# Performance work log

Measured on AMD Instinct MI355X. Metric: run time of the kernel, lower is better.

The kernel has to match this reference:

```python
import jax, jax.numpy as jnp
import numpy as np

N_NODES = 50000
N_EDGES = 500000
D = 128
VOCAB = 10000
OUT = 64
LAYERS = 3
N_GRAPHS = 512


def setup_inputs() -> dict:
    key = jax.random.key(0)
    ks = jax.random.split(key, 10)
    nodes = jax.random.randint(ks[0], (N_NODES,), 0, VOCAB)
    edges = jax.random.randint(ks[1], (2, N_EDGES), 0, N_NODES)
    indices = jax.random.randint(ks[2], (N_NODES,), 0, N_GRAPHS)
    emb = jax.random.normal(ks[3], (VOCAB, D), dtype=jnp.float32) * 0.02
    W0 = jax.random.normal(ks[4], (LAYERS, D, D), dtype=jnp.float32) * (1.0 / np.sqrt(D))
    W1 = jax.random.normal(ks[5], (LAYERS, D, D), dtype=jnp.float32) * (1.0 / np.sqrt(D))
    W2 = jax.random.normal(ks[6], (LAYERS, D, D), dtype=jnp.float32) * (1.0 / np.sqrt(D))
    Wout = jax.random.normal(ks[7], (2 * D, OUT), dtype=jnp.float32) * (1.0 / np.sqrt(2 * D))
    bout = jnp.zeros((OUT,), dtype=jnp.float32)
    return {"nodes": nodes, "edges": edges, "indices": indices, "num_graphs": N_GRAPHS,
            "emb": emb, "W0": W0, "W1": W1, "W2": W2, "Wout": Wout, "bout": bout}


def reference(nodes, edges, indices, num_graphs, emb, W0, W1, W2, Wout, bout):
    n = nodes.shape[0]
    h = emb[nodes]  # [N, D]; Dropout(0.5) is identity in eval mode
    src, dst = edges[0], edges[1]
    seg = jnp.concatenate([dst, src])  # message destinations, [2E]
    deg = jax.ops.segment_sum(jnp.ones_like(seg, dtype=h.dtype), seg, num_segments=n)
    deg = jnp.maximum(deg, 1.0)[:, None]
    for l in range(W0.shape[0]):
        # per-edge linear on gathered endpoints (nn.Linear: x @ W.T)
        m = jnp.concatenate([h[src] @ W1[l].T, h[dst] @ W2[l].T], axis=0)  # [2E, D]
        msg = jax.ops.segment_sum(m, seg, num_segments=n) / deg  # scatter_mean
        h = jax.nn.relu(h @ W0[l].T + msg)
    # graph pooling: scatter_mean + scatter_max
    cnt = jax.ops.segment_sum(jnp.ones((n,), h.dtype), indices, num_segments=num_graphs)
    mean = jax.ops.segment_sum(h, indices, num_segments=num_graphs) / jnp.maximum(cnt, 1.0)[:, None]
    mx = jax.ops.segment_max(h, indices, num_segments=num_graphs)
    mx = jnp.where(jnp.isfinite(mx), mx, 0.0)  # empty segments -> 0 (torch_scatter default)
    v = jnp.concatenate([mean, mx], axis=1)  # [G, 2D]
    return v @ Wout + bout
```

## Files before the change

kernel.cpp:

```cpp
#include <hip/hip_runtime.h>
#include <hip/hip_bf16.h>

#define D 128
#define GRAPHS 512
#define OUTD 64
#define NR 64
#define NSL 16
#define NSCAN (NR * NSL)
#define LRANGE 800

typedef _Float16 half4v __attribute__((ext_vector_type(4)));
typedef _Float16 half8v __attribute__((ext_vector_type(8)));
typedef float float4v __attribute__((ext_vector_type(4)));
typedef float float8v __attribute__((ext_vector_type(8)));
typedef unsigned short u16;

__global__ __launch_bounds__(256) void prep_kernel(
    const int* __restrict__ edges, const int* __restrict__ indices,
    int* __restrict__ pc_in, int* __restrict__ pc_out, int* __restrict__ pc_g,
    const int* __restrict__ nodes, const float* __restrict__ emb,
    _Float16* __restrict__ h,
    const float* __restrict__ W0, const float* __restrict__ W1,
    const float* __restrict__ W2, _Float16* __restrict__ Wpk,
    int E, int n) {
    int tid = threadIdx.x;
    if (blockIdx.x < NSCAN) {
        __shared__ int lin[LRANGE];
        __shared__ int lout[LRANGE];
        int s = blockIdx.x >> 6;
        int r = blockIdx.x & (NR - 1);
        int range = (n + NR - 1) / NR;
        int lo = r * range, hi = min(lo + range, n), len = hi - lo;
        for (int j = tid; j < len; j += 256) { lin[j] = 0; lout[j] = 0; }
        __syncthreads();
        int echunk = (((E + NSL - 1) / NSL) + 3) & ~3;
        int elo = s * echunk, ehi = min(elo + echunk, E);
#define HI(arr, k) { unsigned r_ = (unsigned)((k) - lo); if (r_ < (unsigned)len) atomicAdd(&arr[r_], 1); }
        {
            const int4* s4 = (const int4*)(edges + elo);
            const int4* d4 = (const int4*)(edges + E + elo);
            int m4 = (ehi - elo) >> 2;
            for (int it = tid; it < m4; it += 256) {
                int4 sv = s4[it], dv = d4[it];
                HI(lin, dv.x) HI(lin, dv.y) HI(lin, dv.z) HI(lin, dv.w)
                HI(lout, sv.x) HI(lout, sv.y) HI(lout, sv.z) HI(lout, sv.w)
            }
            for (int e = elo + m4 * 4 + tid; e < ehi; e += 256) {
                HI(lin, edges[E + e])
                HI(lout, edges[e])
            }
        }
#undef HI
        __syncthreads();
        for (int j = tid; j < len; j += 256) {
            pc_in[s * n + lo + j] = lin[j];
            pc_out[s * n + lo + j] = lout[j];
        }
        int grange = (GRAPHS + NR - 1) / NR;
        int glo = r * grange, ghi = min(glo + grange, GRAPHS), glen = ghi - glo;
        __syncthreads();
        for (int j = tid; j < glen; j += 256) lin[j] = 0;
        __syncthreads();
        int ichunk = (((n + NSL - 1) / NSL) + 3) & ~3;
        int ilo = s * ichunk, ihi = min(ilo + ichunk, n);
#define GH(k) { unsigned r_ = (unsigned)((k) - glo); if (r_ < (unsigned)glen) atomicAdd(&lin[r_], 1); }
        {
            const int4* i4 = (const int4*)(indices + ilo);
            int g4 = (ihi - ilo) >> 2;
            for (int it = tid; it < g4; it += 256) {
                int4 v = i4[it];
                GH(v.x) GH(v.y) GH(v.z) GH(v.w)
            }
            for (int e = ilo + g4 * 4 + tid; e < ihi; e += 256) GH(indices[e])
        }
#undef GH
        __syncthreads();
        for (int j = tid; j < glen; j += 256) pc_g[s * GRAPHS + glo + j] = lin[j];
        return;
    }
    int i = (blockIdx.x - NSCAN) * 256 + tid;
    if (i < n * 16) {
        int v = i >> 4, q = i & 15;
        const float4* e4 = (const float4*)emb + (size_t)nodes[v] * 32 + q * 2;
        float4 f0 = e4[0];
        float4 f1 = e4[1];
        half8v o = {(_Float16)f0.x, (_Float16)f0.y, (_Float16)f0.z, (_Float16)f0.w,
                    (_Float16)f1.x, (_Float16)f1.y, (_Float16)f1.z, (_Float16)f1.w};
        ((half8v*)h)[i] = o;
    }
    if (i < 36864) {
        int j4 = (i & 1) * 4;
        int t = i >> 1;
        int lane = t & 63; t >>= 6;
        int nf = t & 7;   t >>= 3;
        int ks = t & 3;   t >>= 2;
        int src = t % 3;
        int l = t / 3;
        const float* W = (src == 0 ? W0 : (src == 1 ? W1 : W2)) + l * D * D;
        int col = nf * 16 + (lane & 15);
        int k = ks * 32 + (lane >> 4) * 8 + j4;
        float4 f = *(const float4*)&W[col * D + k];
        half4v o = {(_Float16)f.x, (_Float16)f.y, (_Float16)f.z, (_Float16)f.w};
        _Float16* dst = Wpk + ((size_t)(((l * 3 + src) * 4 + ks) * 8 + nf) * 64 + lane) * 8 + j4;
        *(half4v*)dst = o;
    }
}

__global__ __launch_bounds__(256) void offsets_kernel(
    const int* __restrict__ pc_in, int* __restrict__ o16_in,
    int* __restrict__ off_in, int* __restrict__ tot_in,
    const int* __restrict__ pc_out, int* __restrict__ o16_out,
    int* __restrict__ off_out, int* __restrict__ tot_out,
    const int* __restrict__ pc_g, int* __restrict__ o16_g,
    int* __restrict__ goff, int* __restrict__ gtot,
    int* totals, int n) {
    __shared__ int ws[8];
    int tid = threadIdx.x;
    int lane = tid & 63, wid = tid >> 6;
    int i = blockIdx.x * 256 + tid;

#define SCAN16(pc, o16, off, tot_arr, total, len)                          \
    do {                                                                   \
        int part_[NSL]; int tot_ = 0;                                      \
        if (i < (len)) {                                                   \
            _Pragma("unroll") for (int k_ = 0; k_ < NSL; ++k_) {           \
                part_[k_] = (pc)[k_ * (len) + i]; tot_ += part_[k_];       \
            }                                                              \
        }                                                                  \
        int v_ = tot_;                                                     \
        _Pragma("unroll") for (int d_ = 1; d_ < 64; d_ <<= 1) {            \
            int t_ = __shfl_up(v_, d_, 64);                                \
            if (lane >= d_) v_ += t_;                                      \
        }                                                                  \
        if (lane == 63) ws[wid] = v_;                                      \
        __syncthreads();                                                   \
        if (tid == 0) {                                                    \
            int s_ = 0;                                                    \
            for (int k_ = 0; k_ < 4; ++k_) { int t_ = ws[k_]; ws[k_] = s_; s_ += t_; } \
            ws[4] = atomicAdd((total), s_);                                \
        }                                                                  \
        __syncthreads();                                                   \
        if (i < (len)) {                                                   \
            int run_ = ws[4] + ws[wid] + v_ - tot_;                        \
            (off)[i] = run_; (tot_arr)[i] = tot_;                          \
            _Pragma("unroll") for (int k_ = 0; k_ < NSL; ++k_) {           \
                (o16)[k_ * (len) + i] = run_; run_ += part_[k_];           \
            }                                                              \
        }                                                                  \
        __syncthreads();                                                   \
    } while (0)

    SCAN16(pc_in, o16_in, off_in, tot_in, &totals[0], n);
    SCAN16(pc_out, o16_out, off_out, tot_out, &totals[1], n);
    if (blockIdx.x < (GRAPHS + 255) / 256)
        SCAN16(pc_g, o16_g, goff, gtot, &totals[2], GRAPHS);
#undef SCAN16
}

__global__ __launch_bounds__(256) void fill_kernel(
    const int* __restrict__ edges, const int* __restrict__ indices,
    const int* __restrict__ o16_in, const int* __restrict__ o16_out,
    const int* __restrict__ o16_g,
    u16* __restrict__ csr_in, u16* __restrict__ csr_out, u16* __restrict__ glist,
    int E, int n) {
    __shared__ int cin[LRANGE];
    __shared__ int cout[LRANGE];
    __shared__ int cg[8];
    int tid = threadIdx.x;
    int s = blockIdx.x >> 6;
    int r = blockIdx.x & (NR - 1);
    int range = (n + NR - 1) / NR;
    int lo = r * range, hi = min(lo + range, n), len = hi - lo;
    int grange = (GRAPHS + NR - 1) / NR;
    int glo = r * grange, ghi = min(glo + grange, GRAPHS), glen = ghi - glo;
    for (int j = tid; j < len; j += 256) {
        cin[j] = o16_in[s * n + lo + j];
        cout[j] = o16_out[s * n + lo + j];
    }
    for (int j = tid; j < glen; j += 256) cg[j] = o16_g[s * GRAPHS + glo + j];
    __syncthreads();

    int echunk = (((E + NSL - 1) / NSL) + 3) & ~3;
    int elo = s * echunk, ehi = min(elo + echunk, E);
#define FIN(k, pay) { unsigned r_ = (unsigned)((k) - lo); if (r_ < (unsigned)len) { \
        int p_ = atomicAdd(&cin[r_], 1); csr_in[p_] = (u16)(pay); } }
#define FOUT(k, pay) { unsigned r_ = (unsigned)((k) - lo); if (r_ < (unsigned)len) { \
        int p_ = atomicAdd(&cout[r_], 1); csr_out[p_] = (u16)(pay); } }
    {
        const int4* s4 = (const int4*)(edges + elo);
        const int4* d4 = (const int4*)(edges + E + elo);
        int m4 = (ehi - elo) >> 2;
        for (int it = tid; it < m4; it += 256) {
            int4 sv = s4[it], dv = d4[it];
            FIN(dv.x, sv.x) FIN(dv.y, sv.y) FIN(dv.z, sv.z) FIN(dv.w, sv.w)
            FOUT(sv.x, dv.x) FOUT(sv.y, dv.y) FOUT(sv.z, dv.z) FOUT(sv.w, dv.w)
        }
        for (int e = elo + m4 * 4 + tid; e < ehi; e += 256) {
            int se = edges[e], de = edges[E + e];
            FIN(de, se)
            FOUT(se, de)
        }
    }
#undef FIN
#undef FOUT
#define FG(g, vv) { unsigned r_ = (unsigned)((g) - glo); if (r_ < (unsigned)glen) { \
        int p_ = atomicAdd(&cg[r_], 1); glist[p_] = (u16)(vv); } }
    {
        int ichunk = (((n + NSL - 1) / NSL) + 3) & ~3;
        int ilo = s * ichunk, ihi = min(ilo + ichunk, n);
        const int4* i4 = (const int4*)(indices + ilo);
        int g4 = (ihi - ilo) >> 2;
        for (int it = tid; it < g4; it += 256) {
            int4 v = i4[it];
            int e = ilo + it * 4;
            FG(v.x, e) FG(v.y, e + 1) FG(v.z, e + 2) FG(v.w, e + 3)
        }
        for (int e = ilo + g4 * 4 + tid; e < ihi; e += 256) FG(indices[e], e)
    }
#undef FG
}

__global__ __launch_bounds__(256) void aggregate_kernel(
    const _Float16* __restrict__ h,
    const u16* __restrict__ csr_in, const int* __restrict__ off_in, const int* __restrict__ cnt_in,
    const u16* __restrict__ csr_out, const int* __restrict__ off_out, const int* __restrict__ cnt_out,
    _Float16* __restrict__ agg1, _Float16* __restrict__ agg2, int n) {
    int grp = threadIdx.x >> 4;
    int lane = threadIdx.x & 15;
    int v = blockIdx.x * 16 + grp;
    if (v >= n) return;
    int s1 = off_in[v], c1 = cnt_in[v];
    int s2 = off_out[v], c2 = cnt_out[v];
    float invd = 1.0f / fmaxf((float)(c1 + c2), 1.0f);
    const half8v* h8 = (const half8v*)h;

    float8v a1 = {0.f, 0.f, 0.f, 0.f, 0.f, 0.f, 0.f, 0.f};
    int i = 0;
    for (; i + 4 <= c1; i += 4) {
        int u0 = csr_in[s1 + i], u1 = csr_in[s1 + i + 1];
        int u2 = csr_in[s1 + i + 2], u3 = csr_in[s1 + i + 3];
        half8v p0 = h8[u0 * 16 + lane];
        half8v p1 = h8[u1 * 16 + lane];
        half8v p2 = h8[u2 * 16 + lane];
        half8v p3 = h8[u3 * 16 + lane];
        a1 += (__builtin_convertvector(p0, float8v) + __builtin_convertvector(p1, float8v)) +
              (__builtin_convertvector(p2, float8v) + __builtin_convertvector(p3, float8v));
    }
    for (; i < c1; ++i)
        a1 += __builtin_convertvector(h8[csr_in[s1 + i] * 16 + lane], float8v);

    float8v a2 = {0.f, 0.f, 0.f, 0.f, 0.f, 0.f, 0.f, 0.f};
    i = 0;
    for (; i + 4 <= c2; i += 4) {
        int u0 = csr_out[s2 + i], u1 = csr_out[s2 + i + 1];
        int u2 = csr_out[s2 + i + 2], u3 = csr_out[s2 + i + 3];
        half8v p0 = h8[u0 * 16 + lane];
        half8v p1 = h8[u1 * 16 + lane];
        half8v p2 = h8[u2 * 16 + lane];
        half8v p3 = h8[u3 * 16 + lane];
        a2 += (__builtin_convertvector(p0, float8v) + __builtin_convertvector(p1, float8v)) +
              (__builtin_convertvector(p2, float8v) + __builtin_convertvector(p3, float8v));
    }
    for (; i < c2; ++i)
        a2 += __builtin_convertvector(h8[csr_out[s2 + i] * 16 + lane], float8v);

    a1 *= invd;
    a2 *= invd;
    ((half8v*)agg1)[v * 16 + lane] = __builtin_convertvector(a1, half8v);
    ((half8v*)agg2)[v * 16 + lane] = __builtin_convertvector(a2, half8v);
}

__global__ __launch_bounds__(128) void transform_mfma(
    const _Float16* __restrict__ Xh, const _Float16* __restrict__ A1,
    const _Float16* __restrict__ A2, const _Float16* __restrict__ Wl,
    _Float16* __restrict__ Hout, int n) {
    __shared__ _Float16 Hs[64][136];
    int tid = threadIdx.x;
    int w = tid >> 6, lane = tid & 63;
    int rbase = blockIdx.x * 64 + w * 32;
    int m0 = lane & 15;
    int kg = lane >> 4;
    int r0 = min(rbase + m0, n - 1);
    int r1 = min(rbase + 16 + m0, n - 1);

    const _Float16* srcs[3] = {Xh, A1, A2};

    float4v acc[2][8];
#pragma unroll
    for (int mf = 0; mf < 2; ++mf)
#pragma unroll
        for (int nf = 0; nf < 8; ++nf) acc[mf][nf] = (float4v){0.f, 0.f, 0.f, 0.f};

#define LOAD_STEP(stp, A0v, A1v, Bv)                                              \
    do {                                                                          \
        const int src_ = (stp) >> 2, ks_ = (stp) & 3;                             \
        const _Float16* X_ = srcs[src_];                                          \
        A0v = *(const half8v*)(X_ + (size_t)r0 * D + ks_ * 32 + kg * 8);          \
        A1v = *(const half8v*)(X_ + (size_t)r1 * D + ks_ * 32 + kg * 8);          \
        const _Float16* wp_ = Wl + (size_t)((src_ * 4 + ks_) * 8) * 512 + lane * 8; \
        _Pragma("unroll") for (int nf_ = 0; nf_ < 8; ++nf_)                       \
            Bv[nf_] = *(const half8v*)(wp_ + nf_ * 512);                          \
    } while (0)

    half8v a0c, a1c, bc[8], a0n, a1n, bn[8];
    LOAD_STEP(0, a0c, a1c, bc);
#pragma unroll
    for (int step = 0; step < 12; ++step) {
        if (step < 11) LOAD_STEP(step + 1, a0n, a1n, bn);
#pragma unroll
        for (int nf = 0; nf < 8; ++nf) {
            acc[0][nf] = __builtin_amdgcn_mfma_f32_16x16x32_f16(a0c, bc[nf], acc[0][nf], 0, 0, 0);
            acc[1][nf] = __builtin_amdgcn_mfma_f32_16x16x32_f16(a1c, bc[nf], acc[1][nf], 0, 0, 0);
        }
        a0c = a0n; a1c = a1n;
#pragma unroll
        for (int nf = 0; nf < 8; ++nf) bc[nf] = bn[nf];
    }
#undef LOAD_STEP

#pragma unroll
    for (int mf = 0; mf < 2; ++mf)
#pragma unroll
        for (int nf = 0; nf < 8; ++nf)
#pragma unroll
            for (int r = 0; r < 4; ++r) {
                int row = w * 32 + mf * 16 + kg * 4 + r;
                int col = nf * 16 + m0;
                Hs[row][col] = (_Float16)fmaxf(acc[mf][nf][r], 0.0f);
            }
    __syncthreads();
#pragma unroll
    for (int it = 0; it < 8; ++it) {
        int id = tid + it * 128;
        int row = id >> 4, c8 = id & 15;
        int grow = blockIdx.x * 64 + row;
        if (grow < n)
            *(half8v*)(Hout + (size_t)grow * D + c8 * 8) = *(const half8v*)&Hs[row][c8 * 8];
    }
}

__global__ __launch_bounds__(128) void pool_head_kernel(
    const _Float16* __restrict__ h, const u16* __restrict__ glist,
    const int* __restrict__ goff, const int* __restrict__ gcnt,
    const float* __restrict__ Wout, const float* __restrict__ bout,
    float* __restrict__ out) {
    __shared__ float feat[2 * D];
    int g = blockIdx.x;
    int t = threadIdx.x;
    int s = goff[g], c = gcnt[g];
    float sum = 0.0f, mx = 0.0f;
    int i = 0;
    for (; i + 4 <= c; i += 4) {
        int v0 = glist[s + i], v1 = glist[s + i + 1];
        int v2 = glist[s + i + 2], v3 = glist[s + i + 3];
        float a = (float)h[(size_t)v0 * D + t];
        float b = (float)h[(size_t)v1 * D + t];
        float cc = (float)h[(size_t)v2 * D + t];
        float d = (float)h[(size_t)v3 * D + t];
        sum += (a + b) + (cc + d);
        mx = fmaxf(mx, fmaxf(fmaxf(a, b), fmaxf(cc, d)));
    }
    for (; i < c; ++i) {
        float a = (float)h[(size_t)glist[s + i] * D + t];
        sum += a;
        mx = fmaxf(mx, a);
    }
    feat[t] = sum / fmaxf((float)c, 1.0f);
    feat[D + t] = mx;
    __syncthreads();
    if (t < OUTD) {
        float acc = bout[t];
#pragma unroll 8
        for (int k = 0; k < 2 * D; ++k)
            acc = fmaf(feat[k], Wout[k * OUTD + t], acc);
        out[g * OUTD + t] = acc;
    }
}

extern "C" void kernel_launch(void* const* d_in, const int* in_sizes, int n_in,
                              void* d_out, int out_size, void* d_ws, size_t ws_size,
                              hipStream_t stream) {
    const int* nodes   = (const int*)d_in[0];
    const int* edges   = (const int*)d_in[1];
    const int* indices = (const int*)d_in[2];
    const float* emb  = (const float*)d_in[4];
    const float* W0   = (const float*)d_in[5];
    const float* W1   = (const float*)d_in[6];
    const float* W2   = (const float*)d_in[7];
    const float* Wout = (const float*)d_in[8];
    const float* bout = (const float*)d_in[9];
    float* out = (float*)d_out;

    const int n = in_sizes[0];
    const int E = in_sizes[1] / 2;

    char* ws = (char*)d_ws;
    size_t off = 0;
    auto alloc = [&](size_t bytes) -> char* {
        char* p = ws + off;
        off = (off + bytes + 255) & ~(size_t)255;
        return p;
    };
    int* totals = (int*)alloc(3 * sizeof(int));
    size_t zbytes = off;
    int* pc_in   = (int*)alloc((size_t)NSL * n * sizeof(int));
    int* pc_out  = (int*)alloc((size_t)NSL * n * sizeof(int));
    int* pc_g    = (int*)alloc(NSL * GRAPHS * sizeof(int));
    int* o16_in  = (int*)alloc((size_t)NSL * n * sizeof(int));
    int* o16_out = (int*)alloc((size_t)NSL * n * sizeof(int));
    int* o16_g   = (int*)alloc(NSL * GRAPHS * sizeof(int));
    int* off_in  = (int*)alloc(n * sizeof(int));
    int* off_out = (int*)alloc(n * sizeof(int));
    int* tot_in  = (int*)alloc(n * sizeof(int));
    int* tot_out = (int*)alloc(n * sizeof(int));
    int* goff    = (int*)alloc(GRAPHS * sizeof(int));
    int* gtot    = (int*)alloc(GRAPHS * sizeof(int));
    u16* glist   = (u16*)alloc(n * sizeof(u16));
    u16* csr_in  = (u16*)alloc(E * sizeof(u16));
    u16* csr_out = (u16*)alloc(E * sizeof(u16));
    _Float16* Wpk = (_Float16*)alloc(3 * 3 * 4 * 8 * 64 * 8 * sizeof(_Float16));
    _Float16* B0 = (_Float16*)alloc((size_t)n * D * sizeof(_Float16));
    _Float16* B1 = (_Float16*)alloc((size_t)n * D * sizeof(_Float16));
    _Float16* B2 = (_Float16*)alloc((size_t)n * D * sizeof(_Float16));
    (void)ws_size;

    hipMemsetAsync(d_ws, 0, zbytes, stream);

    int pblocks = NSCAN + (n * 16 + 255) / 256;
    prep_kernel<<<pblocks, 256, 0, stream>>>(edges, indices, pc_in, pc_out, pc_g,
                                             nodes, emb, B0, W0, W1, W2, Wpk, E, n);
    int oblocks = (n + 255) / 256;
    offsets_kernel<<<oblocks, 256, 0, stream>>>(pc_in, o16_in, off_in, tot_in,
                                                pc_out, o16_out, off_out, tot_out,
                                                pc_g, o16_g, goff, gtot, totals, n);
    fill_kernel<<<NSCAN, 256, 0, stream>>>(edges, indices, o16_in, o16_out, o16_g,
                                           csr_in, csr_out, glist, E, n);

    int ablocks = (n + 15) / 16;
    int tblocks = (n + 63) / 64;
    for (int l = 0; l < 3; ++l) {
        aggregate_kernel<<<ablocks, 256, 0, stream>>>(B0, csr_in, off_in, tot_in,
                                                      csr_out, off_out, tot_out, B1, B2, n);
        transform_mfma<<<tblocks, 128, 0, stream>>>(B0, B1, B2,
                                                    Wpk + (size_t)l * 3 * 4 * 8 * 512,
                                                    B0, n);
    }

    pool_head_kernel<<<GRAPHS, 128, 0, stream>>>(B0, glist, goff, gtot, Wout, bout, out);
}
```

Measured before the change: 315.0 us.

## Fuse neighbor aggregation and MFMA transform into a single per-layer kernel

Merges the aggregation kernel and the MFMA transform kernel into one kernel per layer. Each 64-row block gathers its neighbour means into shared memory and then runs the matmul on them, with the two activation buffers ping-ponged across layers. This removes the global write and re-read of the two aggregate buffers and one launch per layer. In exchange each block does more serial work, uses more shared memory (about 34 KB), and has each wave compute only 16 rows, which may lower occupancy or MFMA efficiency.

New measurement: 328.1 us. 4.2% more time.

```diff
diff --git a/kernel.cpp b/kernel.cpp
--- a/kernel.cpp
+++ b/kernel.cpp
@@ -220,120 +220,118 @@
 #undef FG
 }
 
-__global__ __launch_bounds__(256) void aggregate_kernel(
-    const _Float16* __restrict__ h,
+__global__ __launch_bounds__(256) void fused_layer_kernel(
+    const _Float16* __restrict__ Xin,
     const u16* __restrict__ csr_in, const int* __restrict__ off_in, const int* __restrict__ cnt_in,
     const u16* __restrict__ csr_out, const int* __restrict__ off_out, const int* __restrict__ cnt_out,
-    _Float16* __restrict__ agg1, _Float16* __restrict__ agg2, int n) {
-    int grp = threadIdx.x >> 4;
-    int lane = threadIdx.x & 15;
-    int v = blockIdx.x * 16 + grp;
-    if (v >= n) return;
-    int s1 = off_in[v], c1 = cnt_in[v];
-    int s2 = off_out[v], c2 = cnt_out[v];
-    float invd = 1.0f / fmaxf((float)(c1 + c2), 1.0f);
-    const half8v* h8 = (const half8v*)h;
-
-    float8v a1 = {0.f, 0.f, 0.f, 0.f, 0.f, 0.f, 0.f, 0.f};
-    int i = 0;
-    for (; i + 4 <= c1; i += 4) {
-        int u0 = csr_in[s1 + i], u1 = csr_in[s1 + i + 1];
-        int u2 = csr_in[s1 + i + 2], u3 = csr_in[s1 + i + 3];
-        half8v p0 = h8[u0 * 16 + lane];
-        half8v p1 = h8[u1 * 16 + lane];
-        half8v p2 = h8[u2 * 16 + lane];
-        half8v p3 = h8[u3 * 16 + lane];
-        a1 += (__builtin_convertvector(p0, float8v) + __builtin_convertvector(p1, float8v)) +
-              (__builtin_convertvector(p2, float8v) + __builtin_convertvector(p3, float8v));
-    }
-    for (; i < c1; ++i)
-        a1 += __builtin_convertvector(h8[csr_in[s1 + i] * 16 + lane], float8v);
-
-    float8v a2 = {0.f, 0.f, 0.f, 0.f, 0.f, 0.f, 0.f, 0.f};
-    i = 0;
-    for (; i + 4 <= c2; i += 4) {
-        int u0 = csr_out[s2 + i], u1 = csr_out[s2 + i + 1];
-        int u2 = csr_out[s2 + i + 2], u3 = csr_out[s2 + i + 3];
-        half8v p0 = h8[u0 * 16 + lane];
-        half8v p1 = h8[u1 * 16 + lane];
-        half8v p2 = h8[u2 * 16 + lane];
-        half8v p3 = h8[u3 * 16 + lane];
-        a2 += (__builtin_convertvector(p0, float8v) + __builtin_convertvector(p1, float8v)) +
-              (__builtin_convertvector(p2, float8v) + __builtin_convertvector(p3, float8v));
-    }
-    for (; i < c2; ++i)
-        a2 += __builtin_convertvector(h8[csr_out[s2 + i] * 16 + lane], float8v);
-
-    a1 *= invd;
-    a2 *= invd;
-    ((half8v*)agg1)[v * 16 + lane] = __builtin_convertvector(a1, half8v);
-    ((half8v*)agg2)[v * 16 + lane] = __builtin_convertvector(a2, half8v);
-}
-
-__global__ __launch_bounds__(128) void transform_mfma(
-    const _Float16* __restrict__ Xh, const _Float16* __restrict__ A1,
-    const _Float16* __restrict__ A2, const _Float16* __restrict__ Wl,
+    const _Float16* __restrict__ Wl,
     _Float16* __restrict__ Hout, int n) {
-    __shared__ _Float16 Hs[64][136];
+    __shared__ _Float16 aggL[2][64][136];
     int tid = threadIdx.x;
-    int w = tid >> 6, lane = tid & 63;
-    int rbase = blockIdx.x * 64 + w * 32;
-    int m0 = lane & 15;
-    int kg = lane >> 4;
-    int r0 = min(rbase + m0, n - 1);
-    int r1 = min(rbase + 16 + m0, n - 1);
-
-    const _Float16* srcs[3] = {Xh, A1, A2};
-
-    float4v acc[2][8];
-#pragma unroll
-    for (int mf = 0; mf < 2; ++mf)
-#pragma unroll
-        for (int nf = 0; nf < 8; ++nf) acc[mf][nf] = (float4v){0.f, 0.f, 0.f, 0.f};
-
-#define LOAD_STEP(stp, A0v, A1v, Bv)                                              \
+    int rbase = blockIdx.x * 64;
+
+    {
+        int grp = tid >> 4;
+        int lane = tid & 15;
+        const half8v* h8 = (const half8v*)Xin;
+#pragma unroll
+        for (int p = 0; p < 4; ++p) {
+            int vl = p * 16 + grp;
+            int v = rbase + vl;
+            float8v a1 = {0.f, 0.f, 0.f, 0.f, 0.f, 0.f, 0.f, 0.f};
+            float8v a2 = {0.f, 0.f, 0.f, 0.f, 0.f, 0.f, 0.f, 0.f};
+            float invd = 1.0f;
+            if (v < n) {
+                int s1 = off_in[v], c1 = cnt_in[v];
+                int s2 = off_out[v], c2 = cnt_out[v];
+                invd = 1.0f / fmaxf((float)(c1 + c2), 1.0f);
+                int i = 0;
+                for (; i + 4 <= c1; i += 4) {
+                    int u0 = csr_in[s1 + i], u1 = csr_in[s1 + i + 1];
+                    int u2 = csr_in[s1 + i + 2], u3 = csr_in[s1 + i + 3];
+                    half8v p0 = h8[u0 * 16 + lane];
+                    half8v p1 = h8[u1 * 16 + lane];
+                    half8v p2 = h8[u2 * 16 + lane];
+                    half8v p3 = h8[u3 * 16 + lane];
+                    a1 += (__builtin_convertvector(p0, float8v) + __builtin_convertvector(p1, float8v)) +
+                          (__builtin_convertvector(p2, float8v) + __builtin_convertvector(p3, float8v));
+                }
+                for (; i < c1; ++i)
+                    a1 += __builtin_convertvector(h8[csr_in[s1 + i] * 16 + lane], float8v);
+                i = 0;
+                for (; i + 4 <= c2; i += 4) {
+                    int w0 = csr_out[s2 + i], w1 = csr_out[s2 + i + 1];
+                    int w2 = csr_out[s2 + i + 2], w3 = csr_out[s2 + i + 3];
+                    half8v q0 = h8[w0 * 16 + lane];
+                    half8v q1 = h8[w1 * 16 + lane];
+                    half8v q2 = h8[w2 * 16 + lane];
+                    half8v q3 = h8[w3 * 16 + lane];
+                    a2 += (__builtin_convertvector(q0, float8v) + __builtin_convertvector(q1, float8v)) +
+                          (__builtin_convertvector(q2, float8v) + __builtin_convertvector(q3, float8v));
+                }
+                for (; i < c2; ++i)
+                    a2 += __builtin_convertvector(h8[csr_out[s2 + i] * 16 + lane], float8v);
+            }
+            a1 *= invd;
+            a2 *= invd;
+            *(half8v*)&aggL[0][vl][lane * 8] = __builtin_convertvector(a1, half8v);
+            *(half8v*)&aggL[1][vl][lane * 8] = __builtin_convertvector(a2, half8v);
+        }
+    }
+    __syncthreads();
+
+    int w = tid >> 6, lane64 = tid & 63;
+    int m0 = lane64 & 15;
+    int kg = lane64 >> 4;
+    int rl = w * 16 + m0;
+    int r0 = min(rbase + rl, n - 1);
+
+    float4v acc[8];
+#pragma unroll
+    for (int nf = 0; nf < 8; ++nf) acc[nf] = (float4v){0.f, 0.f, 0.f, 0.f};
+
+#define LOAD_STEP(stp, Av, Bv)                                                    \
     do {                                                                          \
         const int src_ = (stp) >> 2, ks_ = (stp) & 3;                             \
-        const _Float16* X_ = srcs[src_];                                          \
-        A0v = *(const half8v*)(X_ + (size_t)r0 * D + ks_ * 32 + kg * 8);          \
-        A1v = *(const half8v*)(X_ + (size_t)r1 * D + ks_ * 32 + kg * 8);          \
-        const _Float16* wp_ = Wl + (size_t)((src_ * 4 + ks_) * 8) * 512 + lane * 8; \
+        if (src_ == 0)                                                            \
+            Av = *(const half8v*)(Xin + (size_t)r0 * D + ks_ * 32 + kg * 8);      \
+        else                                                                      \
+            Av = *(const half8v*)&aggL[src_ - 1][rl][ks_ * 32 + kg * 8];          \
+        const _Float16* wp_ = Wl + (size_t)((src_ * 4 + ks_) * 8) * 512 + lane64 * 8; \
         _Pragma("unroll") for (int nf_ = 0; nf_ < 8; ++nf_)                       \
             Bv[nf_] = *(const half8v*)(wp_ + nf_ * 512);                          \
     } while (0)
 
-    half8v a0c, a1c, bc[8], a0n, a1n, bn[8];
-    LOAD_STEP(0, a0c, a1c, bc);
+    half8v ac, bc[8], an, bn[8];
+    LOAD_STEP(0, ac, bc);
 #pragma unroll
     for (int step = 0; step < 12; ++step) {
-        if (step < 11) LOAD_STEP(step + 1, a0n, a1n, bn);
-#pragma unroll
-        for (int nf = 0; nf < 8; ++nf) {
-            acc[0][nf] = __builtin_amdgcn_mfma_f32_16x16x32_f16(a0c, bc[nf], acc[0][nf], 0, 0, 0);
-            acc[1][nf] = __builtin_amdgcn_mfma_f32_16x16x32_f16(a1c, bc[nf], acc[1][nf], 0, 0, 0);
-        }
-        a0c = a0n; a1c = a1n;
+        if (step < 11) LOAD_STEP(step + 1, an, bn);
+#pragma unroll
+        for (int nf = 0; nf < 8; ++nf)
+            acc[nf] = __builtin_amdgcn_mfma_f32_16x16x32_f16(ac, bc[nf], acc[nf], 0, 0, 0);
+        ac = an;
 #pragma unroll
         for (int nf = 0; nf < 8; ++nf) bc[nf] = bn[nf];
     }
 #undef LOAD_STEP
 
-#pragma unroll
-    for (int mf = 0; mf < 2; ++mf)
-#pragma unroll
-        for (int nf = 0; nf < 8; ++nf)
-#pragma unroll
-            for (int r = 0; r < 4; ++r) {
-                int row = w * 32 + mf * 16 + kg * 4 + r;
-                int col = nf * 16 + m0;
-                Hs[row][col] = (_Float16)fmaxf(acc[mf][nf][r], 0.0f);
-            }
     __syncthreads();
-#pragma unroll
-    for (int it = 0; it < 8; ++it) {
-        int id = tid + it * 128;
+    _Float16 (*Hs)[136] = aggL[0];
+#pragma unroll
+    for (int nf = 0; nf < 8; ++nf)
+#pragma unroll
+        for (int r = 0; r < 4; ++r) {
+            int row = w * 16 + kg * 4 + r;
+            int col = nf * 16 + m0;
+            Hs[row][col] = (_Float16)fmaxf(acc[nf][r], 0.0f);
+        }
+    __syncthreads();
+#pragma unroll
+    for (int it = 0; it < 4; ++it) {
+        int id = tid + it * 256;
         int row = id >> 4, c8 = id & 15;
-        int grow = blockIdx.x * 64 + row;
+        int grow = rbase + row;
         if (grow < n)
             *(half8v*)(Hout + (size_t)grow * D + c8 * 8) = *(const half8v*)&Hs[row][c8 * 8];
     }
@@ -421,7 +419,6 @@
     _Float16* Wpk = (_Float16*)alloc(3 * 3 * 4 * 8 * 64 * 8 * sizeof(_Float16));
     _Float16* B0 = (_Float16*)alloc((size_t)n * D * sizeof(_Float16));
     _Float16* B1 = (_Float16*)alloc((size_t)n * D * sizeof(_Float16));
-    _Float16* B2 = (_Float16*)alloc((size_t)n * D * sizeof(_Float16));
     (void)ws_size;
 
     hipMemsetAsync(d_ws, 0, zbytes, stream);
@@ -436,15 +433,13 @@
     fill_kernel<<<NSCAN, 256, 0, stream>>>(edges, indices, o16_in, o16_out, o16_g,
                                            csr_in, csr_out, glist, E, n);
 
-    int ablocks = (n + 15) / 16;
-    int tblocks = (n + 63) / 64;
+    int fblocks = (n + 63) / 64;
+    _Float16* Bbuf[2] = {B0, B1};
     for (int l = 0; l < 3; ++l) {
-        aggregate_kernel<<<ablocks, 256, 0, stream>>>(B0, csr_in, off_in, tot_in,
-                                                      csr_out, off_out, tot_out, B1, B2, n);
-        transform_mfma<<<tblocks, 128, 0, stream>>>(B0, B1, B2,
-                                                    Wpk + (size_t)l * 3 * 4 * 8 * 512,
-                                                    B0, n);
-    }
-
-    pool_head_kernel<<<GRAPHS, 128, 0, stream>>>(B0, glist, goff, gtot, Wout, bout, out);
-}
+        fused_layer_kernel<<<fblocks, 256, 0, stream>>>(
+            Bbuf[l & 1], csr_in, off_in, tot_in, csr_out, off_out, tot_out,
+            Wpk + (size_t)l * 3 * 4 * 8 * 512, Bbuf[(l + 1) & 1], n);
+    }
+
+    pool_head_kernel<<<GRAPHS, 128, 0, stream>>>(B1, glist, goff, gtot, Wout, bout, out);
+}
```
